# Kernel tuning notes

Hardware: AMD Instinct MI355X
Metric: run time of the kernel (lower is better)

## Reference

```python
import jax, jax.numpy as jnp
import numpy as np

H = 512   # d_model (hidden)
L = 2     # rnn_layer_dim
E = 321   # enc_in
C = 321   # c_out (must equal enc_in: decoder output is fed back as input)
T = 96    # seq_len
P = 96    # pred_len
B = 512   # batch


def _cell(x, h, c, Wih, Whh, bih, bhh):
    # PyTorch LSTM gate order: input, forget, cell(g), output
    g = x @ Wih.T + h @ Whh.T + bih + bhh
    i, f, gg, o = jnp.split(g, 4, axis=-1)
    c = jax.nn.sigmoid(f) * c + jax.nn.sigmoid(i) * jnp.tanh(gg)
    h = jax.nn.sigmoid(o) * jnp.tanh(c)
    return h, c


def _run_layer(xs, Wih, Whh, bih, bhh):
    # xs: [T, B, in_dim] -> ys: [T, B, H], final (h, c)
    b = xs.shape[1]
    h0 = jnp.zeros((b, Whh.shape[1]), xs.dtype)
    def step(carry, x):
        h, c = carry
        h, c = _cell(x, h, c, Wih, Whh, bih, bhh)
        return (h, c), h
    (h, c), ys = jax.lax.scan(step, (h0, h0), xs)
    return ys, h, c


def _forward(x_enc, x_mark_enc, x_dec, x_mark_dec,
             e_Wih0, e_Whh0, e_bih0, e_bhh0, e_Wih1, e_Whh1, e_bih1, e_bhh1,
             d_Wih0, d_Whh0, d_bih0, d_bhh0, d_Wih1, d_Whh1, d_bih1, d_bhh1,
             fc_W, fc_b):
    del x_mark_enc, x_dec, x_mark_dec  # unused in use_tf=False path
    xs = jnp.swapaxes(x_enc, 0, 1)                     # [T, B, E]
    ys, h0, c0 = _run_layer(xs, e_Wih0, e_Whh0, e_bih0, e_bhh0)
    _,  h1, c1 = _run_layer(ys, e_Wih1, e_Whh1, e_bih1, e_bhh1)

    inp0 = x_enc[:, -1, :]                             # [B, E] last source step

    def dec_step(carry, _):
        inp, h0, c0, h1, c1 = carry
        h0, c0 = _cell(inp, h0, c0, d_Wih0, d_Whh0, d_bih0, d_bhh0)
        h1, c1 = _cell(h0,  h1, c1, d_Wih1, d_Whh1, d_bih1, d_bhh1)
        out = h1 @ fc_W.T + fc_b                       # [B, C]
        return (out, h0, c0, h1, c1), out

    _, outs = jax.lax.scan(dec_step, (inp0, h0, c0, h1, c1), None, length=P)
    return jnp.swapaxes(outs, 0, 1)                    # [B, P, C]


def setup_inputs() -> dict:
    key = jax.random.key(0)
    ks = jax.random.split(key, 24)
    s = 1.0 / np.sqrt(H)  # PyTorch LSTM init scale
    def w(k, shape):
        return jax.random.uniform(k, shape, jnp.float32, -s, s)
    inp = {
        "x_enc": jax.random.normal(ks[0], (B, T, E), jnp.float32),
        "x_mark_enc": jax.random.normal(ks[1], (B, T, 4), jnp.float32),
        "x_dec": jax.random.normal(ks[2], (B, P, C), jnp.float32),
        "x_mark_dec": jax.random.normal(ks[3], (B, P, 4), jnp.float32),
        "e_Wih0": w(ks[4], (4 * H, E)),  "e_Whh0": w(ks[5], (4 * H, H)),
        "e_bih0": w(ks[6], (4 * H,)),    "e_bhh0": w(ks[7], (4 * H,)),
        "e_Wih1": w(ks[8], (4 * H, H)),  "e_Whh1": w(ks[9], (4 * H, H)),
        "e_bih1": w(ks[10], (4 * H,)),   "e_bhh1": w(ks[11], (4 * H,)),
        "d_Wih0": w(ks[12], (4 * H, E)), "d_Whh0": w(ks[13], (4 * H, H)),
        "d_bih0": w(ks[14], (4 * H,)),   "d_bhh0": w(ks[15], (4 * H,)),
        "d_Wih1": w(ks[16], (4 * H, H)), "d_Whh1": w(ks[17], (4 * H, H)),
        "d_bih1": w(ks[18], (4 * H,)),   "d_bhh1": w(ks[19], (4 * H,)),
        "fc_W": w(ks[20], (C, H)),       "fc_b": w(ks[21], (C,)),
    }
    return inp


def reference(x_enc, x_mark_enc, x_dec, x_mark_dec,
              e_Wih0, e_Whh0, e_bih0, e_bhh0, e_Wih1, e_Whh1, e_bih1, e_bhh1,
              d_Wih0, d_Whh0, d_bih0, d_bhh0, d_Wih1, d_Whh1, d_bih1, d_bhh1,
              fc_W, fc_b):
    return _forward(x_enc, x_mark_enc, x_dec, x_mark_dec,
                    e_Wih0, e_Whh0, e_bih0, e_bhh0, e_Wih1, e_Whh1, e_bih1, e_bhh1,
                    d_Wih0, d_Whh0, d_bih0, d_bhh0, d_Wih1, d_Whh1, d_bih1, d_bhh1,
                    fc_W, fc_b)
```

## Files before the change

### kernel.cpp

```cpp
#include <hip/hip_runtime.h>
#include <hip/hip_bf16.h>

#define BB 512
#define TT 96
#define PP 96
#define EE 321
#define CC 321
#define HH 512
#define G4 2048
#define EPAD 352
#define NFC 384

#define BUF_SZ 24576
#define XH_OFF 0
#define XL_OFF 8192
#define WH_OFF 16384
#define WL_OFF 20480
#define FC_SMEM 49152

#define SMEM128 98304
#define DEC_SMEM 65536

typedef unsigned short u16;
typedef __attribute__((ext_vector_type(8))) short bf16x8;
typedef __attribute__((ext_vector_type(16))) float floatx16;

__device__ __forceinline__ void splitf(float v, u16& h, u16& l){
  __hip_bfloat16 bh = __float2bfloat16(v);
  h = *reinterpret_cast<u16*>(&bh);
  float r = v - __bfloat162float(bh);
  __hip_bfloat16 bl = __float2bfloat16(r);
  l = *reinterpret_cast<u16*>(&bl);
}

__device__ __forceinline__ void gload16(const void* g, void* l){
  __builtin_amdgcn_global_load_lds((const __attribute__((address_space(1))) void*)g,
                                   (__attribute__((address_space(3))) void*)l, 16, 0, 0);
}

__global__ void cvt_split(const float* __restrict__ src, u16* __restrict__ hi, u16* __restrict__ lo,
                          int rows, int cols, int rowspad, int colspad){
  int total = rowspad * colspad;
  for (int idx = blockIdx.x * blockDim.x + threadIdx.x; idx < total; idx += gridDim.x * blockDim.x){
    int r = idx / colspad, cc = idx - r * colspad;
    float v = (r < rows && cc < cols) ? src[(size_t)r * cols + cc] : 0.f;
    u16 h, l; splitf(v, h, l);
    hi[idx] = h; lo[idx] = l;
  }
}

__global__ void cvt_bias(const float* __restrict__ b1, const float* __restrict__ b2,
                         float* __restrict__ dst, int n, int npad){
  for (int i = blockIdx.x * blockDim.x + threadIdx.x; i < npad; i += gridDim.x * blockDim.x){
    float v = 0.f;
    if (i < n){ v = b1[i]; if (b2) v += b2[i]; }
    dst[i] = v;
  }
}

__global__ void init_inp(const float* __restrict__ x_enc, u16* __restrict__ inph, u16* __restrict__ inpl){
  int total = BB * EPAD;
  for (int idx = blockIdx.x * blockDim.x + threadIdx.x; idx < total; idx += gridDim.x * blockDim.x){
    int b = idx / EPAD, j = idx - b * EPAD;
    float v = (j < EE) ? x_enc[(size_t)b * TT * EE + (size_t)(TT - 1) * EE + j] : 0.f;
    u16 h, l; splitf(v, h, l);
    inph[idx] = h; inpl[idx] = l;
  }
}

__global__ void split_xenc(const float* __restrict__ x, u16* __restrict__ xh, u16* __restrict__ xl){
  const int total = TT * BB * EPAD;
  for (int idx = blockIdx.x * blockDim.x + threadIdx.x; idx < total; idx += gridDim.x * blockDim.x){
    int e = idx % EPAD;
    int rest = idx / EPAD;
    int b = rest % BB;
    int t = rest / BB;
    float v = (e < EE) ? x[((size_t)b * TT + t) * EE + e] : 0.f;
    u16 h, l; splitf(v, h, l);
    xh[idx] = h; xl[idx] = l;
  }
}

__global__ void wcomb(const float* __restrict__ A, const float* __restrict__ Bm,
                      float* __restrict__ C){
  __shared__ float arow[EE];
  const int g = blockIdx.x;
  for (int e = threadIdx.x; e < EE; e += 256) arow[e] = A[(size_t)g * EE + e];
  __syncthreads();
  for (int k = threadIdx.x; k < HH; k += 256){
    float s = 0.f;
    for (int e = 0; e < EE; ++e) s += arow[e] * Bm[(size_t)e * HH + k];
    C[(size_t)g * HH + k] = s;
  }
}

__global__ void bias_fold(const float* __restrict__ bd0, const float* __restrict__ A,
                          const float* __restrict__ fcb, float* __restrict__ out){
  int g = blockIdx.x * blockDim.x + threadIdx.x;
  if (g < G4){
    float s = bd0[g];
    for (int e = 0; e < EE; ++e) s += A[(size_t)g * EE + e] * fcb[e];
    out[g] = s;
  }
}

template<int MT>
__device__ __forceinline__ void lstm_body(
    char* smem, int bx,
    const u16* __restrict__ Xh, const u16* __restrict__ Xl, int K1pad,
    const u16* __restrict__ Wih_h, const u16* __restrict__ Wih_l,
    const u16* __restrict__ Whh_h, const u16* __restrict__ Whh_l,
    const float* __restrict__ bias, const float* __restrict__ Gin,
    const u16* __restrict__ Hph, const u16* __restrict__ Hpl,
    u16* __restrict__ Hnh, u16* __restrict__ Hnl,
    float* __restrict__ cst)
{
  constexpr int XROWB = MT * 64;
  constexpr int BUFB  = 2 * XROWB + 8192;
  constexpr int WH_O  = 2 * XROWB;
  constexpr int WL_O  = 2 * XROWB + 4096;

  float (*sG)[68] = (float (*)[68])(smem);

  const int tid  = threadIdx.x;
  const int lane = tid & 63;
  const int wid  = tid >> 6;
  const int wm = wid >> 1, wn = wid & 1;
  const int m0 = (bx >> 5) * MT;
  const int u0 = (bx & 31) * 16;

  floatx16 acc0 = {0.f,0.f,0.f,0.f,0.f,0.f,0.f,0.f,0.f,0.f,0.f,0.f,0.f,0.f,0.f,0.f};
  floatx16 acc1 = acc0;

  const int ml    = lane & 31;
  const int thalf = lane >> 5;
  const int a0r = (MT == 128 ? wm * 64 : wm * 32) + ml;
  const int a1r = a0r + 32;
  const int brw = wn * 32 + ml;
  const int xa  = (a0r >> 1) & 3;
  const int xb  = (brw >> 1) & 3;

  const int sl  = lane & 3;
  const int rq  = lane >> 2;
  const int rx0 = wid * (MT / 4) + rq;
  const int rw  = wid * 16 + rq;
  const int sgx = (sl ^ ((rx0 >> 1) & 3)) << 4;
  const int sgw = (sl ^ ((rw  >> 1) & 3)) << 4;
  const size_t gxr0 = (size_t)(m0 + rx0);
  const size_t gxr1 = gxr0 + 16;
  const size_t gwr  = (size_t)wid * HH + u0 + rq;
  const int oX = wid * (MT / 4) * 64;
  const int oW = wid * 16 * 64;

  const int nch1 = K1pad >> 5;
  const int ncht = Hph ? nch1 + (HH >> 5) : nch1;

  auto stage = [&](int ch){
    const bool p1 = ch < nch1;
    const int k0 = (p1 ? ch : ch - nch1) << 5;
    const u16* xh = p1 ? Xh : Hph;
    const u16* xl = p1 ? Xl : Hpl;
    const u16* wh = p1 ? Wih_h : Whh_h;
    const u16* wl = p1 ? Wih_l : Whh_l;
    const size_t Kp = p1 ? (size_t)K1pad : (size_t)HH;
    char* b = smem + (ch & 3) * BUFB;
    gload16((const char*)(xh + gxr0 * Kp + k0) + sgx, b + oX);
    if constexpr (MT == 128) gload16((const char*)(xh + gxr1 * Kp + k0) + sgx, b + oX + 1024);
    gload16((const char*)(xl + gxr0 * Kp + k0) + sgx, b + XROWB + oX);
    if constexpr (MT == 128) gload16((const char*)(xl + gxr1 * Kp + k0) + sgx, b + XROWB + oX + 1024);
    gload16((const char*)(wh + gwr  * Kp + k0) + sgw, b + WH_O + oW);
    gload16((const char*)(wl + gwr  * Kp + k0) + sgw, b + WL_O + oW);
  };

  stage(0); stage(1); stage(2);
  for (int ch = 0; ch < ncht; ++ch){
    const int rem = (ncht - 1 - ch) < 2 ? (ncht - 1 - ch) : 2;
    __builtin_amdgcn_sched_barrier(0);
    if constexpr (MT == 128){
      if      (rem == 2) asm volatile("s_waitcnt vmcnt(12)" ::: "memory");
      else if (rem == 1) asm volatile("s_waitcnt vmcnt(6)"  ::: "memory");
      else               asm volatile("s_waitcnt vmcnt(0)"  ::: "memory");
    } else {
      if      (rem == 2) asm volatile("s_waitcnt vmcnt(8)"  ::: "memory");
      else if (rem == 1) asm volatile("s_waitcnt vmcnt(4)"  ::: "memory");
      else               asm volatile("s_waitcnt vmcnt(0)"  ::: "memory");
    }
    asm volatile("s_waitcnt lgkmcnt(0)" ::: "memory");
    __builtin_amdgcn_s_barrier();
    __builtin_amdgcn_sched_barrier(0);
    if (ch + 3 < ncht) stage(ch + 3);
    const char* bufc = smem + (ch & 3) * BUFB;
    #pragma unroll
    for (int kk2 = 0; kk2 < 2; ++kk2){
      const int t0 = kk2 * 2 + thalf;
      bf16x8 ah0 = *(const bf16x8*)(bufc + a0r * 64 + ((t0 ^ xa) << 4));
      bf16x8 al0 = *(const bf16x8*)(bufc + XROWB + a0r * 64 + ((t0 ^ xa) << 4));
      bf16x8 bh  = *(const bf16x8*)(bufc + WH_O + brw * 64 + ((t0 ^ xb) << 4));
      bf16x8 bl  = *(const bf16x8*)(bufc + WL_O + brw * 64 + ((t0 ^ xb) << 4));
      acc0 = __builtin_amdgcn_mfma_f32_32x32x16_bf16(ah0, bh, acc0, 0, 0, 0);
      acc0 = __builtin_amdgcn_mfma_f32_32x32x16_bf16(ah0, bl, acc0, 0, 0, 0);
      acc0 = __builtin_amdgcn_mfma_f32_32x32x16_bf16(al0, bh, acc0, 0, 0, 0);
      if constexpr (MT == 128){
        bf16x8 ah1 = *(const bf16x8*)(bufc + a1r * 64 + ((t0 ^ xa) << 4));
        bf16x8 al1 = *(const bf16x8*)(bufc + XROWB + a1r * 64 + ((t0 ^ xa) << 4));
        acc1 = __builtin_amdgcn_mfma_f32_32x32x16_bf16(ah1, bh, acc1, 0, 0, 0);
        acc1 = __builtin_amdgcn_mfma_f32_32x32x16_bf16(ah1, bl, acc1, 0, 0, 0);
        acc1 = __builtin_amdgcn_mfma_f32_32x32x16_bf16(al1, bh, acc1, 0, 0, 0);
      }
    }
  }
  __syncthreads();

  #pragma unroll
  for (int r = 0; r < 16; ++r){
    const int mm = (r & 3) + 8 * (r >> 2) + 4 * thalf;
    if constexpr (MT == 128){
      sG[wm * 64 + mm][wn * 32 + ml]      = acc0[r];
      sG[wm * 64 + 32 + mm][wn * 32 + ml] = acc1[r];
    } else {
      sG[wm * 32 + mm][wn * 32 + ml]      = acc0[r];
    }
  }
  __syncthreads();
  for (int e = tid; e < MT * 16; e += 256){
    const int m = e >> 4, u = e & 15;
    const int gj = u0 + u;
    float gi = sG[m][u]      + bias[gj];
    float gf = sG[m][16 + u] + bias[HH + gj];
    float gg = sG[m][32 + u] + bias[2 * HH + gj];
    float go = sG[m][48 + u] + bias[3 * HH + gj];
    if (Gin){
      const float* gb = Gin + (size_t)(m0 + m) * G4;
      gi += gb[gj]; gf += gb[HH + gj]; gg += gb[2 * HH + gj]; go += gb[3 * HH + gj];
    }
    const float si = 1.f / (1.f + expf(-gi));
    const float sf = 1.f / (1.f + expf(-gf));
    const float so = 1.f / (1.f + expf(-go));
    const size_t sidx = (size_t)(m0 + m) * HH + gj;
    const float cn = sf * cst[sidx] + si * tanhf(gg);
    const float hn = so * tanhf(cn);
    cst[sidx] = cn;
    u16 hh, hl; splitf(hn, hh, hl);
    Hnh[sidx] = hh; Hnl[sidx] = hl;
  }
}

__device__ __forceinline__ void part_body(
    char* smem, int bx,
    const u16* __restrict__ Xh, const u16* __restrict__ Xl,
    const u16* __restrict__ W_h, const u16* __restrict__ W_l,
    float* __restrict__ Gout)
{
  constexpr int XROWB = 64 * 64;
  constexpr int BUFB  = 2 * XROWB + 8192;
  constexpr int WH_O  = 2 * XROWB;
  constexpr int WL_O  = 2 * XROWB + 4096;

  const int tid  = threadIdx.x;
  const int lane = tid & 63;
  const int wid  = tid >> 6;
  const int wm = wid >> 1, wn = wid & 1;
  const int m0 = (bx >> 5) * 64;
  const int u0 = (bx & 31) * 16;

  floatx16 acc0 = {0.f,0.f,0.f,0.f,0.f,0.f,0.f,0.f,0.f,0.f,0.f,0.f,0.f,0.f,0.f,0.f};

  const int ml    = lane & 31;
  const int thalf = lane >> 5;
  const int a0r = wm * 32 + ml;
  const int brw = wn * 32 + ml;
  const int xa  = (a0r >> 1) & 3;
  const int xb  = (brw >> 1) & 3;

  const int sl  = lane & 3;
  const int rq  = lane >> 2;
  const int rx0 = wid * 16 + rq;
  const int rw  = wid * 16 + rq;
  const int sgx = (sl ^ ((rx0 >> 1) & 3)) << 4;
  const int sgw = (sl ^ ((rw  >> 1) & 3)) << 4;
  const size_t gxr0 = (size_t)(m0 + rx0);
  const size_t gwr  = (size_t)wid * HH + u0 + rq;
  const int oX = wid * 16 * 64;
  const int oW = wid * 16 * 64;

  auto stage = [&](int ch){
    const int k0 = ch << 5;
    char* b = smem + (ch & 3) * BUFB;
    gload16((const char*)(Xh + gxr0 * HH + k0) + sgx, b + oX);
    gload16((const char*)(Xl + gxr0 * HH + k0) + sgx, b + XROWB + oX);
    gload16((const char*)(W_h + gwr * HH + k0) + sgw, b + WH_O + oW);
    gload16((const char*)(W_l + gwr * HH + k0) + sgw, b + WL_O + oW);
  };

  stage(0); stage(1); stage(2);
  for (int ch = 0; ch < 16; ++ch){
    const int rem = (15 - ch) < 2 ? (15 - ch) : 2;
    __builtin_amdgcn_sched_barrier(0);
    if      (rem == 2) asm volatile("s_waitcnt vmcnt(8)" ::: "memory");
    else if (rem == 1) asm volatile("s_waitcnt vmcnt(4)" ::: "memory");
    else               asm volatile("s_waitcnt vmcnt(0)" ::: "memory");
    asm volatile("s_waitcnt lgkmcnt(0)" ::: "memory");
    __builtin_amdgcn_s_barrier();
    __builtin_amdgcn_sched_barrier(0);
    if (ch + 3 < 16) stage(ch + 3);
    const char* bufc = smem + (ch & 3) * BUFB;
    #pragma unroll
    for (int kk2 = 0; kk2 < 2; ++kk2){
      const int t0 = kk2 * 2 + thalf;
      bf16x8 ah0 = *(const bf16x8*)(bufc + a0r * 64 + ((t0 ^ xa) << 4));
      bf16x8 al0 = *(const bf16x8*)(bufc + XROWB + a0r * 64 + ((t0 ^ xa) << 4));
      bf16x8 bh  = *(const bf16x8*)(bufc + WH_O + brw * 64 + ((t0 ^ xb) << 4));
      bf16x8 bl  = *(const bf16x8*)(bufc + WL_O + brw * 64 + ((t0 ^ xb) << 4));
      acc0 = __builtin_amdgcn_mfma_f32_32x32x16_bf16(ah0, bh, acc0, 0, 0, 0);
      acc0 = __builtin_amdgcn_mfma_f32_32x32x16_bf16(ah0, bl, acc0, 0, 0, 0);
      acc0 = __builtin_amdgcn_mfma_f32_32x32x16_bf16(al0, bh, acc0, 0, 0, 0);
    }
  }
  const int c = wn * 32 + ml;
  const size_t gcolo = (size_t)(c >> 4) * HH + u0 + (c & 15);
  #pragma unroll
  for (int r = 0; r < 16; ++r){
    const int mm = (r & 3) + 8 * (r >> 2) + 4 * thalf;
    Gout[(size_t)(m0 + wm * 32 + mm) * G4 + gcolo] = acc0[r];
  }
}

__global__ __launch_bounds__(256) void dec_ab(
    const u16* Xfh, const u16* Xfl, int Kf,
    const u16* Wf_h, const u16* Wf_l,
    const float* bias, const float* Gin,
    u16* Hnh, u16* Hnl, float* cst,
    const u16* Xph, const u16* Xpl,
    const u16* Wp_h, const u16* Wp_l,
    float* Gout)
{
  extern __shared__ char smem[];
  if (blockIdx.x < 256)
    lstm_body<64>(smem, blockIdx.x, Xfh, Xfl, Kf, Wf_h, Wf_l, nullptr, nullptr,
                  bias, Gin, nullptr, nullptr, Hnh, Hnl, cst);
  else
    part_body(smem, blockIdx.x - 256, Xph, Xpl, Wp_h, Wp_l, Gout);
}

__global__ __launch_bounds__(256) void part_only(
    const u16* Xh, const u16* Xl, const u16* W_h, const u16* W_l, float* Gout)
{
  extern __shared__ char smem[];
  part_body(smem, blockIdx.x, Xh, Xl, W_h, W_l, Gout);
}

__global__ __launch_bounds__(256) void lstm_pair(
    int act0, const u16* X0h, const u16* X0l,
    const u16* W0ih_h, const u16* W0ih_l, const u16* W0hh_h, const u16* W0hh_l,
    const float* b0, const u16* H0ph, const u16* H0pl, u16* H0nh, u16* H0nl, float* c0,
    int act1, const u16* X1h, const u16* X1l,
    const u16* W1ih_h, const u16* W1ih_l, const u16* W1hh_h, const u16* W1hh_l,
    const float* b1, const u16* H1ph, const u16* H1pl, u16* H1nh, u16* H1nl, float* c1)
{
  extern __shared__ char smem[];
  const int half = blockIdx.x >> 7;
  const int bx   = blockIdx.x & 127;
  if (half == 0 ? !act0 : !act1) return;
  lstm_body<128>(smem, bx,
                 half ? X1h : X0h, half ? X1l : X0l, half ? HH : EPAD,
                 half ? W1ih_h : W0ih_h, half ? W1ih_l : W0ih_l,
                 half ? W1hh_h : W0hh_h, half ? W1hh_l : W0hh_l,
                 half ? b1 : b0, nullptr,
                 half ? H1ph : H0ph, half ? H1pl : H0pl,
                 half ? H1nh : H0nh, half ? H1nl : H0nl,
                 half ? c1 : c0);
}

__global__ __launch_bounds__(256) void fc_batch(
    const u16* __restrict__ Hh, const u16* __restrict__ Hl,
    const u16* __restrict__ Wh, const u16* __restrict__ Wl,
    const float* __restrict__ bfc,
    float* __restrict__ out)
{
  extern __shared__ char smem[];
  const int tid = threadIdx.x, lane = tid & 63, wid = tid >> 6;
  const int wm = wid >> 1, wn = wid & 1;
  const int m0 = blockIdx.x * 128;
  const int n0 = blockIdx.y * 64;

  floatx16 acc0 = {0.f,0.f,0.f,0.f,0.f,0.f,0.f,0.f,0.f,0.f,0.f,0.f,0.f,0.f,0.f,0.f};
  floatx16 acc1 = {0.f,0.f,0.f,0.f,0.f,0.f,0.f,0.f,0.f,0.f,0.f,0.f,0.f,0.f,0.f,0.f};

  const int ml    = lane & 31;
  const int thalf = lane >> 5;
  const int a0r = wm * 64 + ml;
  const int a1r = a0r + 32;
  const int brw = wn * 32 + ml;
  const int xa  = (a0r >> 1) & 3;
  const int xb  = (brw >> 1) & 3;

  const int sl  = lane & 3;
  const int rq  = lane >> 2;
  const int rx0 = wid * 32 + rq;
  const int rw  = wid * 16 + rq;
  const int sgx = (sl ^ ((rx0 >> 1) & 3)) << 4;
  const int sgw = (sl ^ ((rw  >> 1) & 3)) << 4;
  const size_t gxr0 = (size_t)(m0 + rx0);
  const size_t gxr1 = gxr0 + 16;
  const size_t gwr  = (size_t)(n0 + rw);
  const int oX = wid * 32 * 64;
  const int oW = wid * 16 * 64;

  auto stage = [&](int ch){
    const int k0 = ch << 5;
    char* b = smem + (ch & 1) * BUF_SZ;
    gload16((const char*)(Hh + gxr0 * HH + k0) + sgx, b + XH_OFF + oX);
    gload16((const char*)(Hh + gxr1 * HH + k0) + sgx, b + XH_OFF + oX + 1024);
    gload16((const char*)(Hl + gxr0 * HH + k0) + sgx, b + XL_OFF + oX);
    gload16((const char*)(Hl + gxr1 * HH + k0) + sgx, b + XL_OFF + oX + 1024);
    gload16((const char*)(Wh + gwr  * HH + k0) + sgw, b + WH_OFF + oW);
    gload16((const char*)(Wl + gwr  * HH + k0) + sgw, b + WL_OFF + oW);
  };

  stage(0);
  for (int ch = 0; ch < 16; ++ch){
    if (ch + 1 < 16) stage(ch + 1);
    __builtin_amdgcn_sched_barrier(0);
    if (ch + 1 < 16) { asm volatile("s_waitcnt vmcnt(6)" ::: "memory"); }
    else             { asm volatile("s_waitcnt vmcnt(0)" ::: "memory"); }
    __builtin_amdgcn_s_barrier();
    __builtin_amdgcn_sched_barrier(0);
    const char* bufc = smem + (ch & 1) * BUF_SZ;
    #pragma unroll
    for (int kk2 = 0; kk2 < 2; ++kk2){
      const int t0 = kk2 * 2 + thalf;
      bf16x8 ah0 = *(const bf16x8*)(bufc + XH_OFF + a0r * 64 + ((t0 ^ xa) << 4));
      bf16x8 al0 = *(const bf16x8*)(bufc + XL_OFF + a0r * 64 + ((t0 ^ xa) << 4));
      bf16x8 ah1 = *(const bf16x8*)(bufc + XH_OFF + a1r * 64 + ((t0 ^ xa) << 4));
      bf16x8 al1 = *(const bf16x8*)(bufc + XL_OFF + a1r * 64 + ((t0 ^ xa) << 4));
      bf16x8 bh  = *(const bf16x8*)(bufc + WH_OFF + brw * 64 + ((t0 ^ xb) << 4));
      bf16x8 bl  = *(const bf16x8*)(bufc + WL_OFF + brw * 64 + ((t0 ^ xb) << 4));
      acc0 = __builtin_amdgcn_mfma_f32_32x32x16_bf16(ah0, bh, acc0, 0, 0, 0);
      acc0 = __builtin_amdgcn_mfma_f32_32x32x16_bf16(ah0, bl, acc0, 0, 0, 0);
      acc0 = __builtin_amdgcn_mfma_f32_32x32x16_bf16(al0, bh, acc0, 0, 0, 0);
      acc1 = __builtin_amdgcn_mfma_f32_32x32x16_bf16(ah1, bh, acc1, 0, 0, 0);
      acc1 = __builtin_amdgcn_mfma_f32_32x32x16_bf16(ah1, bl, acc1, 0, 0, 0);
      acc1 = __builtin_amdgcn_mfma_f32_32x32x16_bf16(al1, bh, acc1, 0, 0, 0);
    }
    __builtin_amdgcn_sched_barrier(0);
    asm volatile("s_waitcnt lgkmcnt(0)" ::: "memory");
    __builtin_amdgcn_s_barrier();
    __builtin_amdgcn_sched_barrier(0);
  }

  const int n = n0 + wn * 32 + ml;
  if (n < CC){
    const float bv = bfc[n];
    #pragma unroll
    for (int r = 0; r < 16; ++r){
      const int mm = (r & 3) + 8 * (r >> 2) + 4 * thalf;
      {
        const int rr = m0 + wm * 64 + mm;
        out[(size_t)(rr & 511) * PP * CC + (size_t)(rr >> 9) * CC + n] = acc0[r] + bv;
      }
      {
        const int rr = m0 + wm * 64 + 32 + mm;
        out[(size_t)(rr & 511) * PP * CC + (size_t)(rr >> 9) * CC + n] = acc1[r] + bv;
      }
    }
  }
}

extern "C" void kernel_launch(void* const* d_in, const int* in_sizes, int n_in,
                              void* d_out, int out_size, void* d_ws, size_t ws_size,
                              hipStream_t stream) {
  const float* x_enc  = (const float*)d_in[0];
  const float* e_Wih0 = (const float*)d_in[4];
  const float* e_Whh0 = (const float*)d_in[5];
  const float* e_bih0 = (const float*)d_in[6];
  const float* e_bhh0 = (const float*)d_in[7];
  const float* e_Wih1 = (const float*)d_in[8];
  const float* e_Whh1 = (const float*)d_in[9];
  const float* e_bih1 = (const float*)d_in[10];
  const float* e_bhh1 = (const float*)d_in[11];
  const float* d_Wih0 = (const float*)d_in[12];
  const float* d_Whh0 = (const float*)d_in[13];
  const float* d_bih0 = (const float*)d_in[14];
  const float* d_bhh0 = (const float*)d_in[15];
  const float* d_Wih1 = (const float*)d_in[16];
  const float* d_Whh1 = (const float*)d_in[17];
  const float* d_bih1 = (const float*)d_in[18];
  const float* d_bhh1 = (const float*)d_in[19];
  const float* fc_W   = (const float*)d_in[20];
  const float* fc_b   = (const float*)d_in[21];

  static bool attr_done = false;
  if (!attr_done){
    hipFuncSetAttribute((const void*)lstm_pair, hipFuncAttributeMaxDynamicSharedMemorySize, SMEM128);
    hipFuncSetAttribute((const void*)dec_ab,    hipFuncAttributeMaxDynamicSharedMemorySize, DEC_SMEM);
    hipFuncSetAttribute((const void*)part_only, hipFuncAttributeMaxDynamicSharedMemorySize, DEC_SMEM);
    attr_done = true;
  }

  char* base = (char*)d_ws;
  size_t off = 0;
  auto alloc_us = [&](size_t n){ u16* p = (u16*)(base + off); off += ((n * 2 + 15) & ~(size_t)15); return p; };
  auto alloc_f  = [&](size_t n){ float* p = (float*)(base + off); off += ((n * 4 + 15) & ~(size_t)15); return p; };

  u16 *We0ih_h = alloc_us((size_t)G4 * EPAD), *We0ih_l = alloc_us((size_t)G4 * EPAD);
  u16 *We0hh_h = alloc_us((size_t)G4 * HH),   *We0hh_l = alloc_us((size_t)G4 * HH);
  u16 *We1ih_h = alloc_us((size_t)G4 * HH),   *We1ih_l = alloc_us((size_t)G4 * HH);
  u16 *We1hh_h = alloc_us((size_t)G4 * HH),   *We1hh_l = alloc_us((size_t)G4 * HH);
  u16 *Wd0ih_h = alloc_us((size_t)G4 * EPAD), *Wd0ih_l = alloc_us((size_t)G4 * EPAD);
  u16 *Wd0hh_h = alloc_us((size_t)G4 * HH),   *Wd0hh_l = alloc_us((size_t)G4 * HH);
  u16 *Wd1ih_h = alloc_us((size_t)G4 * HH),   *Wd1ih_l = alloc_us((size_t)G4 * HH);
  u16 *Wd1hh_h = alloc_us((size_t)G4 * HH),   *Wd1hh_l = alloc_us((size_t)G4 * HH);
  u16 *Wfc_h   = alloc_us((size_t)NFC * HH),  *Wfc_l   = alloc_us((size_t)NFC * HH);
  u16 *Wc_h    = alloc_us((size_t)G4 * HH),   *Wc_l    = alloc_us((size_t)G4 * HH);
  float* be0 = alloc_f(G4);
  float* be1 = alloc_f(G4);
  float* bd0 = alloc_f(G4);
  float* bd1 = alloc_f(G4);
  float* bfc = alloc_f(NFC);
  float* bd0c = alloc_f(G4);
  float* Wcf32 = alloc_f((size_t)G4 * HH);
  float* Gp0 = alloc_f((size_t)BB * G4);
  float* Gp1 = alloc_f((size_t)BB * G4);
  u16* h0h[2]; u16* h0l[2]; u16* h1h[2]; u16* h1l[2];
  h0h[0] = alloc_us((size_t)BB * HH); h0l[0] = alloc_us((size_t)BB * HH);
  h1h[0] = alloc_us((size_t)BB * HH); h1l[0] = alloc_us((size_t)BB * HH);
  float* c0 = alloc_f((size_t)BB * HH);
  float* c1 = alloc_f((size_t)BB * HH);
  h0h[1] = alloc_us((size_t)BB * HH); h0l[1] = alloc_us((size_t)BB * HH);
  h1h[1] = alloc_us((size_t)BB * HH); h1l[1] = alloc_us((size_t)BB * HH);
  u16* inph = alloc_us((size_t)BB * EPAD);
  u16* inpl = alloc_us((size_t)BB * EPAD);
  u16* Xench = alloc_us((size_t)TT * BB * EPAD);
  u16* Xencl = alloc_us((size_t)TT * BB * EPAD);
  u16* histh = alloc_us((size_t)PP * BB * HH);
  u16* histl = alloc_us((size_t)PP * BB * HH);

  cvt_split<<<512, 256, 0, stream>>>(e_Wih0, We0ih_h, We0ih_l, G4, EE, G4, EPAD);
  cvt_split<<<512, 256, 0, stream>>>(e_Whh0, We0hh_h, We0hh_l, G4, HH, G4, HH);
  cvt_split<<<512, 256, 0, stream>>>(e_Wih1, We1ih_h, We1ih_l, G4, HH, G4, HH);
  cvt_split<<<512, 256, 0, stream>>>(e_Whh1, We1hh_h, We1hh_l, G4, HH, G4, HH);
  cvt_split<<<512, 256, 0, stream>>>(d_Wih0, Wd0ih_h, Wd0ih_l, G4, EE, G4, EPAD);
  cvt_split<<<512, 256, 0, stream>>>(d_Whh0, Wd0hh_h, Wd0hh_l, G4, HH, G4, HH);
  cvt_split<<<512, 256, 0, stream>>>(d_Wih1, Wd1ih_h, Wd1ih_l, G4, HH, G4, HH);
  cvt_split<<<512, 256, 0, stream>>>(d_Whh1, Wd1hh_h, Wd1hh_l, G4, HH, G4, HH);
  cvt_split<<<512, 256, 0, stream>>>(fc_W,   Wfc_h,   Wfc_l,   CC, HH, NFC, HH);
  cvt_bias<<<8, 256, 0, stream>>>(e_bih0, e_bhh0, be0, G4, G4);
  cvt_bias<<<8, 256, 0, stream>>>(e_bih1, e_bhh1, be1, G4, G4);
  cvt_bias<<<8, 256, 0, stream>>>(d_bih0, d_bhh0, bd0, G4, G4);
  cvt_bias<<<8, 256, 0, stream>>>(d_bih1, d_bhh1, bd1, G4, G4);
  cvt_bias<<<2, 256, 0, stream>>>(fc_b, nullptr, bfc, CC, NFC);
  wcomb<<<G4, 256, 0, stream>>>(d_Wih0, fc_W, Wcf32);
  bias_fold<<<8, 256, 0, stream>>>(bd0, d_Wih0, fc_b, bd0c);
  cvt_split<<<512, 256, 0, stream>>>(Wcf32, Wc_h, Wc_l, G4, HH, G4, HH);
  hipMemsetAsync(h0h[0], 0, (size_t)4 * BB * HH * sizeof(u16) + (size_t)2 * BB * HH * sizeof(float), stream);
  init_inp<<<512, 256, 0, stream>>>(x_enc, inph, inpl);
  split_xenc<<<4096, 256, 0, stream>>>(x_enc, Xench, Xencl);

  for (int t = 0; t <= TT; ++t){
    const int rd = t & 1, wrp = (t + 1) & 1;
    const size_t ts = (size_t)(t < TT ? t : 0) * BB * EPAD;
    lstm_pair<<<256, 256, SMEM128, stream>>>(
        (t < TT) ? 1 : 0, Xench + ts, Xencl + ts,
        We0ih_h, We0ih_l, We0hh_h, We0hh_l, be0,
        h0h[rd], h0l[rd], h0h[wrp], h0l[wrp], c0,
        (t > 0) ? 1 : 0, h0h[rd], h0l[rd],
        We1ih_h, We1ih_l, We1hh_h, We1hh_l, be1,
        h1h[wrp], h1l[wrp], h1h[rd], h1l[rd], c1);
  }

  const size_t S = (size_t)BB * HH;
  part_only<<<256, 256, DEC_SMEM, stream>>>(h0h[0], h0l[0], Wd0hh_h, Wd0hh_l, Gp0);
  for (int p = 0; p < PP; ++p){
    const u16* hp_h = p ? histh + (size_t)(p - 1) * S : h1h[0];
    const u16* hp_l = p ? histl + (size_t)(p - 1) * S : h1l[0];
    dec_ab<<<512, 256, DEC_SMEM, stream>>>(
        p ? hp_h : inph, p ? hp_l : inpl, p ? HH : EPAD,
        p ? Wc_h : Wd0ih_h, p ? Wc_l : Wd0ih_l,
        p ? bd0c : bd0, Gp0,
        h0h[1], h0l[1], c0,
        hp_h, hp_l, Wd1hh_h, Wd1hh_l, Gp1);
    dec_ab<<<512, 256, DEC_SMEM, stream>>>(
        h0h[1], h0l[1], HH,
        Wd1ih_h, Wd1ih_l,
        bd1, Gp1,
        histh + (size_t)p * S, histl + (size_t)p * S, c1,
        h0h[1], h0l[1], Wd0hh_h, Wd0hh_l, Gp0);
  }

  fc_batch<<<dim3((PP * BB) / 128, NFC / 64), 256, FC_SMEM, stream>>>(
      histh, histl, Wfc_h, Wfc_l, bfc, (float*)d_out);
}
```

Before: 5.869 ms.

## Fuse setup kernels and shrink encoder LSTM tiles to 64 rows for more blocks

The nine weight-split launches become one multi-job kernel. The bias-sum, input-split and x_enc-split kernels are merged into a single prep kernel, and the combined decoder weight is now computed, split to bf16 hi/lo and bias-folded in one kernel, which removes the fp32 intermediate buffer. The encoder lstm_pair now uses 64-row M tiles with 512 blocks and half the shared memory, and it and dec_ab get launch_bounds(256,2) to allow two blocks per CU. This trades fewer launches and better occupancy for smaller per-block tiles with less weight reuse, and the fused prep does serial per-job loops.

Result: faster. 5.714 ms (-2.6%).

```diff
diff --git a/kernel.cpp b/kernel.cpp
--- a/kernel.cpp
+++ b/kernel.cpp
@@ -18,7 +18,6 @@
 #define WL_OFF 20480
 #define FC_SMEM 49152
 
-#define SMEM128 98304
 #define DEC_SMEM 65536
 
 typedef unsigned short u16;
@@ -38,69 +37,81 @@
                                    (__attribute__((address_space(3))) void*)l, 16, 0, 0);
 }
 
-__global__ void cvt_split(const float* __restrict__ src, u16* __restrict__ hi, u16* __restrict__ lo,
-                          int rows, int cols, int rowspad, int colspad){
-  int total = rowspad * colspad;
-  for (int idx = blockIdx.x * blockDim.x + threadIdx.x; idx < total; idx += gridDim.x * blockDim.x){
-    int r = idx / colspad, cc = idx - r * colspad;
-    float v = (r < rows && cc < cols) ? src[(size_t)r * cols + cc] : 0.f;
-    u16 h, l; splitf(v, h, l);
-    hi[idx] = h; lo[idx] = l;
-  }
-}
-
-__global__ void cvt_bias(const float* __restrict__ b1, const float* __restrict__ b2,
-                         float* __restrict__ dst, int n, int npad){
-  for (int i = blockIdx.x * blockDim.x + threadIdx.x; i < npad; i += gridDim.x * blockDim.x){
-    float v = 0.f;
-    if (i < n){ v = b1[i]; if (b2) v += b2[i]; }
-    dst[i] = v;
-  }
-}
-
-__global__ void init_inp(const float* __restrict__ x_enc, u16* __restrict__ inph, u16* __restrict__ inpl){
-  int total = BB * EPAD;
-  for (int idx = blockIdx.x * blockDim.x + threadIdx.x; idx < total; idx += gridDim.x * blockDim.x){
+struct SJob { const float* src; u16* hi; u16* lo; int rows, cols, rowspad, colspad; };
+struct SJobs { SJob j[9]; };
+
+__global__ void split_multi(SJobs js){
+  const int stride = gridDim.x * blockDim.x;
+  const int t0 = blockIdx.x * blockDim.x + threadIdx.x;
+  for (int k = 0; k < 9; ++k){
+    const SJob J = js.j[k];
+    const int total = J.rowspad * J.colspad;
+    for (int idx = t0; idx < total; idx += stride){
+      int r = idx / J.colspad, cc = idx - r * J.colspad;
+      float v = (r < J.rows && cc < J.cols) ? J.src[(size_t)r * J.cols + cc] : 0.f;
+      u16 h, l; splitf(v, h, l);
+      J.hi[idx] = h; J.lo[idx] = l;
+    }
+  }
+}
+
+__global__ void wcomb_fused(const float* __restrict__ A,
+                            const float* __restrict__ Bm,
+                            const float* __restrict__ bih, const float* __restrict__ bhh,
+                            const float* __restrict__ fcb,
+                            u16* __restrict__ Wc_h, u16* __restrict__ Wc_l,
+                            float* __restrict__ bd0c){
+  __shared__ float arow[EE];
+  __shared__ float red[256];
+  const int g = blockIdx.x;
+  for (int e = threadIdx.x; e < EE; e += 256) arow[e] = A[(size_t)g * EE + e];
+  __syncthreads();
+  float ps = 0.f;
+  for (int e = threadIdx.x; e < EE; e += 256) ps += arow[e] * fcb[e];
+  red[threadIdx.x] = ps; __syncthreads();
+  for (int s = 128; s > 0; s >>= 1){
+    if (threadIdx.x < s) red[threadIdx.x] += red[threadIdx.x + s];
+    __syncthreads();
+  }
+  if (threadIdx.x == 0) bd0c[g] = bih[g] + bhh[g] + red[0];
+  for (int k = threadIdx.x; k < HH; k += 256){
+    float s = 0.f;
+    for (int e = 0; e < EE; ++e) s += arow[e] * Bm[(size_t)e * HH + k];
+    u16 h, l; splitf(s, h, l);
+    Wc_h[(size_t)g * HH + k] = h; Wc_l[(size_t)g * HH + k] = l;
+  }
+}
+
+__global__ void prep_misc(
+    const float* e_bih0, const float* e_bhh0, float* be0,
+    const float* e_bih1, const float* e_bhh1, float* be1,
+    const float* d_bih0, const float* d_bhh0, float* bd0,
+    const float* d_bih1, const float* d_bhh1, float* bd1,
+    const float* fc_b, float* bfc,
+    const float* x_enc, u16* inph, u16* inpl, u16* xh, u16* xl){
+  const int stride = gridDim.x * blockDim.x;
+  const int t0 = blockIdx.x * blockDim.x + threadIdx.x;
+  for (int i = t0; i < G4; i += stride){
+    be0[i] = e_bih0[i] + e_bhh0[i];
+    be1[i] = e_bih1[i] + e_bhh1[i];
+    bd0[i] = d_bih0[i] + d_bhh0[i];
+    bd1[i] = d_bih1[i] + d_bhh1[i];
+  }
+  for (int i = t0; i < NFC; i += stride) bfc[i] = (i < CC) ? fc_b[i] : 0.f;
+  for (int idx = t0; idx < BB * EPAD; idx += stride){
     int b = idx / EPAD, j = idx - b * EPAD;
     float v = (j < EE) ? x_enc[(size_t)b * TT * EE + (size_t)(TT - 1) * EE + j] : 0.f;
     u16 h, l; splitf(v, h, l);
     inph[idx] = h; inpl[idx] = l;
   }
-}
-
-__global__ void split_xenc(const float* __restrict__ x, u16* __restrict__ xh, u16* __restrict__ xl){
-  const int total = TT * BB * EPAD;
-  for (int idx = blockIdx.x * blockDim.x + threadIdx.x; idx < total; idx += gridDim.x * blockDim.x){
+  for (int idx = t0; idx < TT * BB * EPAD; idx += stride){
     int e = idx % EPAD;
     int rest = idx / EPAD;
     int b = rest % BB;
     int t = rest / BB;
-    float v = (e < EE) ? x[((size_t)b * TT + t) * EE + e] : 0.f;
+    float v = (e < EE) ? x_enc[((size_t)b * TT + t) * EE + e] : 0.f;
     u16 h, l; splitf(v, h, l);
     xh[idx] = h; xl[idx] = l;
-  }
-}
-
-__global__ void wcomb(const float* __restrict__ A, const float* __restrict__ Bm,
-                      float* __restrict__ C){
-  __shared__ float arow[EE];
-  const int g = blockIdx.x;
-  for (int e = threadIdx.x; e < EE; e += 256) arow[e] = A[(size_t)g * EE + e];
-  __syncthreads();
-  for (int k = threadIdx.x; k < HH; k += 256){
-    float s = 0.f;
-    for (int e = 0; e < EE; ++e) s += arow[e] * Bm[(size_t)e * HH + k];
-    C[(size_t)g * HH + k] = s;
-  }
-}
-
-__global__ void bias_fold(const float* __restrict__ bd0, const float* __restrict__ A,
-                          const float* __restrict__ fcb, float* __restrict__ out){
-  int g = blockIdx.x * blockDim.x + threadIdx.x;
-  if (g < G4){
-    float s = bd0[g];
-    for (int e = 0; e < EE; ++e) s += A[(size_t)g * EE + e] * fcb[e];
-    out[g] = s;
   }
 }
 
@@ -325,7 +336,14 @@
   }
 }
 
-__global__ __launch_bounds__(256) void dec_ab(
+__global__ __launch_bounds__(256) void part_only(
+    const u16* Xh, const u16* Xl, const u16* W_h, const u16* W_l, float* Gout)
+{
+  extern __shared__ char smem[];
+  part_body(smem, blockIdx.x, Xh, Xl, W_h, W_l, Gout);
+}
+
+__global__ __launch_bounds__(256, 2) void dec_ab(
     const u16* Xfh, const u16* Xfl, int Kf,
     const u16* Wf_h, const u16* Wf_l,
     const float* bias, const float* Gin,
@@ -342,14 +360,7 @@
     part_body(smem, blockIdx.x - 256, Xph, Xpl, Wp_h, Wp_l, Gout);
 }
 
-__global__ __launch_bounds__(256) void part_only(
-    const u16* Xh, const u16* Xl, const u16* W_h, const u16* W_l, float* Gout)
-{
-  extern __shared__ char smem[];
-  part_body(smem, blockIdx.x, Xh, Xl, W_h, W_l, Gout);
-}
-
-__global__ __launch_bounds__(256) void lstm_pair(
+__global__ __launch_bounds__(256, 2) void lstm_pair(
     int act0, const u16* X0h, const u16* X0l,
     const u16* W0ih_h, const u16* W0ih_l, const u16* W0hh_h, const u16* W0hh_l,
     const float* b0, const u16* H0ph, const u16* H0pl, u16* H0nh, u16* H0nl, float* c0,
@@ -358,17 +369,17 @@
     const float* b1, const u16* H1ph, const u16* H1pl, u16* H1nh, u16* H1nl, float* c1)
 {
   extern __shared__ char smem[];
-  const int half = blockIdx.x >> 7;
-  const int bx   = blockIdx.x & 127;
+  const int half = blockIdx.x >> 8;
+  const int bx   = blockIdx.x & 255;
   if (half == 0 ? !act0 : !act1) return;
-  lstm_body<128>(smem, bx,
-                 half ? X1h : X0h, half ? X1l : X0l, half ? HH : EPAD,
-                 half ? W1ih_h : W0ih_h, half ? W1ih_l : W0ih_l,
-                 half ? W1hh_h : W0hh_h, half ? W1hh_l : W0hh_l,
-                 half ? b1 : b0, nullptr,
-                 half ? H1ph : H0ph, half ? H1pl : H0pl,
-                 half ? H1nh : H0nh, half ? H1nl : H0nl,
-                 half ? c1 : c0);
+  lstm_body<64>(smem, bx,
+                half ? X1h : X0h, half ? X1l : X0l, half ? HH : EPAD,
+                half ? W1ih_h : W0ih_h, half ? W1ih_l : W0ih_l,
+                half ? W1hh_h : W0hh_h, half ? W1hh_l : W0hh_l,
+                half ? b1 : b0, nullptr,
+                half ? H1ph : H0ph, half ? H1pl : H0pl,
+                half ? H1nh : H0nh, half ? H1nl : H0nl,
+                half ? c1 : c0);
 }
 
 __global__ __launch_bounds__(256) void fc_batch(
@@ -491,9 +502,9 @@
 
   static bool attr_done = false;
   if (!attr_done){
-    hipFuncSetAttribute((const void*)lstm_pair, hipFuncAttributeMaxDynamicSharedMemorySize, SMEM128);
+    hipFuncSetAttribute((const void*)lstm_pair, hipFuncAttributeMaxDynamicSharedMemorySize, DEC_SMEM);
+    hipFuncSetAttribute((const void*)part_only, hipFuncAttributeMaxDynamicSharedMemorySize, DEC_SMEM);
     hipFuncSetAttribute((const void*)dec_ab,    hipFuncAttributeMaxDynamicSharedMemorySize, DEC_SMEM);
-    hipFuncSetAttribute((const void*)part_only, hipFuncAttributeMaxDynamicSharedMemorySize, DEC_SMEM);
     attr_done = true;
   }
 
@@ -518,7 +529,6 @@
   float* bd1 = alloc_f(G4);
   float* bfc = alloc_f(NFC);
   float* bd0c = alloc_f(G4);
-  float* Wcf32 = alloc_f((size_t)G4 * HH);
   float* Gp0 = alloc_f((size_t)BB * G4);
   float* Gp1 = alloc_f((size_t)BB * G4);
   u16* h0h[2]; u16* h0l[2]; u16* h1h[2]; u16* h1l[2];
@@ -535,31 +545,31 @@
   u16* histh = alloc_us((size_t)PP * BB * HH);
   u16* histl = alloc_us((size_t)PP * BB * HH);
 
-  cvt_split<<<512, 256, 0, stream>>>(e_Wih0, We0ih_h, We0ih_l, G4, EE, G4, EPAD);
-  cvt_split<<<512, 256, 0, stream>>>(e_Whh0, We0hh_h, We0hh_l, G4, HH, G4, HH);
-  cvt_split<<<512, 256, 0, stream>>>(e_Wih1, We1ih_h, We1ih_l, G4, HH, G4, HH);
-  cvt_split<<<512, 256, 0, stream>>>(e_Whh1, We1hh_h, We1hh_l, G4, HH, G4, HH);
-  cvt_split<<<512, 256, 0, stream>>>(d_Wih0, Wd0ih_h, Wd0ih_l, G4, EE, G4, EPAD);
-  cvt_split<<<512, 256, 0, stream>>>(d_Whh0, Wd0hh_h, Wd0hh_l, G4, HH, G4, HH);
-  cvt_split<<<512, 256, 0, stream>>>(d_Wih1, Wd1ih_h, Wd1ih_l, G4, HH, G4, HH);
-  cvt_split<<<512, 256, 0, stream>>>(d_Whh1, Wd1hh_h, Wd1hh_l, G4, HH, G4, HH);
-  cvt_split<<<512, 256, 0, stream>>>(fc_W,   Wfc_h,   Wfc_l,   CC, HH, NFC, HH);
-  cvt_bias<<<8, 256, 0, stream>>>(e_bih0, e_bhh0, be0, G4, G4);
-  cvt_bias<<<8, 256, 0, stream>>>(e_bih1, e_bhh1, be1, G4, G4);
-  cvt_bias<<<8, 256, 0, stream>>>(d_bih0, d_bhh0, bd0, G4, G4);
-  cvt_bias<<<8, 256, 0, stream>>>(d_bih1, d_bhh1, bd1, G4, G4);
-  cvt_bias<<<2, 256, 0, stream>>>(fc_b, nullptr, bfc, CC, NFC);
-  wcomb<<<G4, 256, 0, stream>>>(d_Wih0, fc_W, Wcf32);
-  bias_fold<<<8, 256, 0, stream>>>(bd0, d_Wih0, fc_b, bd0c);
-  cvt_split<<<512, 256, 0, stream>>>(Wcf32, Wc_h, Wc_l, G4, HH, G4, HH);
+  {
+    SJobs js = {{
+      { e_Wih0, We0ih_h, We0ih_l, G4, EE, G4, EPAD },
+      { e_Whh0, We0hh_h, We0hh_l, G4, HH, G4, HH },
+      { e_Wih1, We1ih_h, We1ih_l, G4, HH, G4, HH },
+      { e_Whh1, We1hh_h, We1hh_l, G4, HH, G4, HH },
+      { d_Wih0, Wd0ih_h, Wd0ih_l, G4, EE, G4, EPAD },
+      { d_Whh0, Wd0hh_h, Wd0hh_l, G4, HH, G4, HH },
+      { d_Wih1, Wd1ih_h, Wd1ih_l, G4, HH, G4, HH },
+      { d_Whh1, Wd1hh_h, Wd1hh_l, G4, HH, G4, HH },
+      { fc_W,   Wfc_h,   Wfc_l,   CC, HH, NFC, HH },
+    }};
+    split_multi<<<1024, 256, 0, stream>>>(js);
+  }
+  wcomb_fused<<<G4, 256, 0, stream>>>(d_Wih0, fc_W, d_bih0, d_bhh0, fc_b, Wc_h, Wc_l, bd0c);
+  prep_misc<<<2048, 256, 0, stream>>>(
+      e_bih0, e_bhh0, be0, e_bih1, e_bhh1, be1,
+      d_bih0, d_bhh0, bd0, d_bih1, d_bhh1, bd1,
+      fc_b, bfc, x_enc, inph, inpl, Xench, Xencl);
   hipMemsetAsync(h0h[0], 0, (size_t)4 * BB * HH * sizeof(u16) + (size_t)2 * BB * HH * sizeof(float), stream);
-  init_inp<<<512, 256, 0, stream>>>(x_enc, inph, inpl);
-  split_xenc<<<4096, 256, 0, stream>>>(x_enc, Xench, Xencl);
 
   for (int t = 0; t <= TT; ++t){
     const int rd = t & 1, wrp = (t + 1) & 1;
     const size_t ts = (size_t)(t < TT ? t : 0) * BB * EPAD;
-    lstm_pair<<<256, 256, SMEM128, stream>>>(
+    lstm_pair<<<512, 256, DEC_SMEM, stream>>>(
         (t < TT) ? 1 : 0, Xench + ts, Xencl + ts,
         We0ih_h, We0ih_l, We0hh_h, We0hh_l, be0,
         h0h[rd], h0l[rd], h0h[wrp], h0l[wrp], c0,
```
